# Kernel tuning notes

Measured on AMD Instinct MI355X. Metric: run time of the kernel, lower is better.

## Reference

```python
import jax, jax.numpy as jnp
import numpy as np

M, K, N = 4096, 4096, 11008


def setup_inputs() -> dict:
    key = jax.random.key(0)
    k1, k2, k3 = jax.random.split(key, 3)
    x = jax.random.normal(k1, (M, K), dtype=jnp.float16)
    weight_packed = jax.random.randint(k2, ((K + 1) // 2, N), 0, 256, dtype=jnp.int32)
    weight_scale = jax.random.uniform(k3, (N,), dtype=jnp.float32) * 0.05 + 1e-3
    return {"x": x, "weight_packed": weight_packed, "weight_scale": weight_scale}


def reference(x, weight_packed, weight_scale):
    # Unpack int4 nibbles: low nibble -> even K index, high nibble -> odd K index.
    packed = weight_packed.astype(jnp.uint8)                      # [K//2, N]
    low = (packed & 15).astype(jnp.float32) - 8.0                 # even rows
    high = ((packed >> 4) & 15).astype(jnp.float32) - 8.0         # odd rows
    k = x.shape[-1]
    w = jnp.stack([low, high], axis=1).reshape(-1, low.shape[1])[:k]  # [K, N]
    # Per-output-feature symmetric scale, then fp16 GEMM (matches torch fallback).
    w = (w * weight_scale[None, :]).astype(jnp.float16)
    out = jnp.matmul(x, w)                                        # [M, N] fp16
    return out
```

## Files before the change

kernel.cpp:

```cpp
#include <hip/hip_runtime.h>
#include <hip/hip_fp16.h>
#include <stdint.h>


#define M_DIM 4096
#define K_DIM 4096
#define N_DIM 11008
#define KH    (K_DIM / 2)

#define WS_XH_BYTES  ((size_t)M_DIM * K_DIM * 2)

typedef __attribute__((ext_vector_type(8))) _Float16 f16x8;
typedef __attribute__((ext_vector_type(2))) _Float16 h2;
typedef __attribute__((ext_vector_type(4))) float f32x4;
typedef unsigned short ushortx;

__device__ __forceinline__ unsigned pack_f16_pair(float lo, float hi) {
    return __builtin_bit_cast(unsigned, __builtin_amdgcn_cvt_pkrtz(lo, hi));
}

__device__ __forceinline__ unsigned dq_pair(unsigned v) {
    unsigned c = (v & 0xFu) | ((v << 12) & 0x000F0000u) | 0x64006400u;
    h2 r = __builtin_bit_cast(h2, c) + __builtin_bit_cast(h2, 0xE408E408u);
    return __builtin_bit_cast(unsigned, r);
}

__device__ __forceinline__ void gld_lds16(const void* g, void* l) {
    __builtin_amdgcn_global_load_lds(
        (const __attribute__((address_space(1))) unsigned int*)g,
        (__attribute__((address_space(3))) unsigned int*)l,
        16, 0, 0);
}

__global__ void __launch_bounds__(256) cvt_x_kernel(
    const float* __restrict__ X, unsigned short* __restrict__ Xh)
{
    size_t i = ((size_t)blockIdx.x * 256 + threadIdx.x) * 8;
    float4 a = *(const float4*)(X + i);
    float4 b = *(const float4*)(X + i + 4);
    uint4 o = make_uint4(pack_f16_pair(a.x, a.y), pack_f16_pair(a.z, a.w),
                         pack_f16_pair(b.x, b.y), pack_f16_pair(b.z, b.w));
    *(uint4*)(Xh + i) = o;
}

__global__ void __launch_bounds__(256) dqt_kernel(
    const int* __restrict__ WP, unsigned* __restrict__ Wt)
{
    __shared__ unsigned Lt[64][65];
    const int t = threadIdx.x;
    const int n0 = blockIdx.x * 64;
    const int r0 = blockIdx.y * 64;
    const int g = t >> 6, l = t & 63;
#pragma unroll
    for (int i = 0; i < 16; ++i) {
        const int r = r0 + g * 16 + i;
        Lt[l][g * 16 + i] = dq_pair((unsigned)WP[(size_t)r * N_DIM + n0 + l]);
    }
    __syncthreads();
    const int nr = t >> 2, sg = t & 3;
    unsigned* dst = Wt + (size_t)(n0 + nr) * KH + r0 + sg * 16;
#pragma unroll
    for (int c = 0; c < 4; ++c) {
        uint4 v = make_uint4(Lt[nr][sg * 16 + c * 4 + 0], Lt[nr][sg * 16 + c * 4 + 1],
                             Lt[nr][sg * 16 + c * 4 + 2], Lt[nr][sg * 16 + c * 4 + 3]);
        *(uint4*)(dst + c * 4) = v;
    }
}

__global__ void __launch_bounds__(512, 2) qgemm6_kernel(
    const unsigned short* __restrict__ Xh,
    const unsigned*       __restrict__ Wt,
    const float*          __restrict__ WS,
    float*                __restrict__ Out)
{
    __shared__ unsigned short LA[2][2][8192];
    __shared__ unsigned short LB[2][2][8192];

    const int t = threadIdx.x;
    const int w = t >> 6;
    const int l = t & 63;

    const int bid = blockIdx.x;
    const int wg  = (bid & 7) * 86 + (bid >> 3);
    const int by  = wg / 43;
    const int bx  = wg - by * 43;
    const int bm0 = by * 256;
    const int bn0 = bx * 256;

    const int wr = w >> 2;
    const int wc = w & 3;

    f32x4 acc[8][4];
#pragma unroll
    for (int i = 0; i < 8; ++i)
#pragma unroll
        for (int j = 0; j < 4; ++j)
            acc[i][j] = (f32x4){0.f, 0.f, 0.f, 0.f};

    const int cS = (t & 7) ^ ((t >> 3) & 7);
    const unsigned short* gA0 = Xh + (size_t)(bm0 + (t >> 3)) * K_DIM + cS * 8;
    const unsigned*       gB0 = Wt + (size_t)(bn0 + (t >> 3)) * KH + cS * 4;
    const int t8 = t * 8;

#define STAGE_A(buf, h, kt) do {                                              \
    gld_lds16(gA0 + (size_t)((h) * 128) * K_DIM + (size_t)(kt) * 64,          \
              &LA[buf][h][t8]);                                               \
    gld_lds16(gA0 + (size_t)((h) * 128 + 64) * K_DIM + (size_t)(kt) * 64,     \
              &LA[buf][h][4096 + t8]);                                        \
} while (0)

#define STAGE_B(buf, h, kt) do {                                              \
    gld_lds16(gB0 + (size_t)((h) * 128) * KH + (size_t)(kt) * 32,             \
              &LB[buf][h][t8]);                                               \
    gld_lds16(gB0 + (size_t)((h) * 128 + 64) * KH + (size_t)(kt) * 32,        \
              &LB[buf][h][4096 + t8]);                                        \
} while (0)

    const int lq = l >> 4;
    const int lr = l & 15;

    f16x8 bf[4][2];

#define LOAD_BF(buf) do {                                                     \
    _Pragma("unroll")                                                         \
    for (int ni = 0; ni < 4; ++ni) {                                          \
        const int rrow = (wc & 1) * 64 + ni * 16 + lr;                        \
        _Pragma("unroll")                                                     \
        for (int ks = 0; ks < 2; ++ks)                                        \
            bf[ni][ks] = *(const f16x8*)                                      \
                &LB[buf][wc >> 1][rrow * 64 + ((ks * 4 + lq) ^ (rrow & 7)) * 8]; \
    }                                                                         \
} while (0)

#define MFMA_PH(buf, p) do {                                                  \
    f16x8 _af[2][2];                                                          \
    _Pragma("unroll")                                                         \
    for (int mi2 = 0; mi2 < 2; ++mi2) {                                       \
        const int rrow = (2 * (p) + mi2) * 16 + lr;                           \
        _Pragma("unroll")                                                     \
        for (int ks = 0; ks < 2; ++ks)                                        \
            _af[mi2][ks] = *(const f16x8*)                                    \
                &LA[buf][wr][rrow * 64 + ((ks * 4 + lq) ^ (rrow & 7)) * 8];   \
    }                                                                         \
    __builtin_amdgcn_s_setprio(1);                                            \
    _Pragma("unroll")                                                         \
    for (int mi2 = 0; mi2 < 2; ++mi2)                                         \
        _Pragma("unroll")                                                     \
        for (int ni = 0; ni < 4; ++ni)                                        \
            _Pragma("unroll")                                                 \
            for (int ks = 0; ks < 2; ++ks)                                    \
                acc[2 * (p) + mi2][ni] = __builtin_amdgcn_mfma_f32_16x16x32_f16( \
                    _af[mi2][ks], bf[ni][ks], acc[2 * (p) + mi2][ni], 0, 0, 0); \
    __builtin_amdgcn_s_setprio(0);                                            \
} while (0)

#define WAITV(n) asm volatile("s_waitcnt vmcnt(" #n ")" ::: "memory")
#define BAR()    do { asm volatile("" ::: "memory");                          \
                      __builtin_amdgcn_s_barrier();                           \
                      asm volatile("" ::: "memory"); } while (0)

    const int NT = K_DIM / 64;

    STAGE_A(0, 0, 0); STAGE_A(0, 1, 0);
    STAGE_B(0, 0, 0); STAGE_B(0, 1, 0);

    for (int i = 0; i < 31; ++i) {
        const int t1 = 2 * i + 1, t2 = 2 * i + 2;
        BAR(); STAGE_A(1, 0, t1); WAITV(2); BAR();
        LOAD_BF(0); MFMA_PH(0, 0);
        STAGE_A(1, 1, t1); MFMA_PH(0, 1);
        STAGE_B(1, 0, t1); MFMA_PH(0, 2);
        STAGE_B(1, 1, t1); MFMA_PH(0, 3);
        BAR(); STAGE_A(0, 0, t2); WAITV(2); BAR();
        LOAD_BF(1); MFMA_PH(1, 0);
        STAGE_A(0, 1, t2); MFMA_PH(1, 1);
        STAGE_B(0, 0, t2); MFMA_PH(1, 2);
        STAGE_B(0, 1, t2); MFMA_PH(1, 3);
    }
    {
        BAR(); STAGE_A(1, 0, 63); WAITV(2); BAR();
        LOAD_BF(0); MFMA_PH(0, 0);
        STAGE_A(1, 1, 63); MFMA_PH(0, 1);
        STAGE_B(1, 0, 63); MFMA_PH(0, 2);
        STAGE_B(1, 1, 63); MFMA_PH(0, 3);
        BAR(); WAITV(0); BAR();
        LOAD_BF(1); MFMA_PH(1, 0);
        MFMA_PH(1, 1);
        MFMA_PH(1, 2);
        MFMA_PH(1, 3);
    }

#pragma unroll
    for (int ni = 0; ni < 4; ++ni) {
        const int col = bn0 + wc * 64 + ni * 16 + lr;
        const float s = WS[col];
#pragma unroll
        for (int mi = 0; mi < 8; ++mi) {
            const int row = bm0 + wr * 128 + mi * 16 + lq * 4;
#pragma unroll
            for (int i = 0; i < 4; ++i) {
                Out[(size_t)(row + i) * N_DIM + col] = acc[mi][ni][i] * s;
            }
        }
    }
#undef STAGE_A
#undef STAGE_B
#undef LOAD_BF
#undef MFMA_PH
#undef WAITV
#undef BAR
}

extern "C" void kernel_launch(void* const* d_in, const int* in_sizes, int n_in,
                              void* d_out, int out_size, void* d_ws, size_t ws_size,
                              hipStream_t stream) {
    const float* X  = (const float*)d_in[0];
    const int*   WP = (const int*)d_in[1];
    const float* WS = (const float*)d_in[2];
    float*       Out = (float*)d_out;

    unsigned short* Xh = (unsigned short*)d_ws;
    unsigned*       Wt = (unsigned*)((char*)d_ws + WS_XH_BYTES);

    cvt_x_kernel<<<(M_DIM * K_DIM) / (256 * 8), 256, 0, stream>>>(X, Xh);
    dim3 gdq(N_DIM / 64, KH / 64);
    dqt_kernel<<<gdq, 256, 0, stream>>>(WP, Wt);
    dim3 grid((N_DIM / 256) * (M_DIM / 256));
    qgemm6_kernel<<<grid, 512, 0, stream>>>(Xh, Wt, WS, Out);
}
```

Baseline: 475.4 us.

## Restructure GEMM main loop into quadrant MFMA schedule with barrier-interleaved loads

Replaces the four-phase MFMA loop with a quadrant schedule. Each wave loads A and B fragments for half-tiles and issues 16 MFMAs per quadrant, separated by barriers and explicit lgkmcnt waits. Global-to-LDS loads are split into finer chunks placed between quadrants. The block-to-tile mapping also changes so that each XCD owns two M-rows of tiles, which is meant to improve L2 reuse of A. The extra barriers add synchronisation overhead, and the new mapping changes how much B is shared per XCD.

```diff
diff --git a/kernel.cpp b/kernel.cpp
--- a/kernel.cpp
+++ b/kernel.cpp
@@ -13,7 +13,6 @@
 typedef __attribute__((ext_vector_type(8))) _Float16 f16x8;
 typedef __attribute__((ext_vector_type(2))) _Float16 h2;
 typedef __attribute__((ext_vector_type(4))) float f32x4;
-typedef unsigned short ushortx;
 
 __device__ __forceinline__ unsigned pack_f16_pair(float lo, float hi) {
     return __builtin_bit_cast(unsigned, __builtin_amdgcn_cvt_pkrtz(lo, hi));
@@ -67,7 +66,7 @@
     }
 }
 
-__global__ void __launch_bounds__(512, 2) qgemm6_kernel(
+__global__ void __launch_bounds__(512, 2) qgemm7_kernel(
     const unsigned short* __restrict__ Xh,
     const unsigned*       __restrict__ Wt,
     const float*          __restrict__ WS,
@@ -81,9 +80,10 @@
     const int l = t & 63;
 
     const int bid = blockIdx.x;
-    const int wg  = (bid & 7) * 86 + (bid >> 3);
-    const int by  = wg / 43;
-    const int bx  = wg - by * 43;
+    const int xcd = bid & 7;
+    const int i8  = bid >> 3;
+    const int bx  = i8 >> 1;
+    const int by  = (xcd << 1) | (i8 & 1);
     const int bm0 = by * 256;
     const int bn0 = bx * 256;
 
@@ -102,93 +102,106 @@
     const unsigned*       gB0 = Wt + (size_t)(bn0 + (t >> 3)) * KH + cS * 4;
     const int t8 = t * 8;
 
-#define STAGE_A(buf, h, kt) do {                                              \
-    gld_lds16(gA0 + (size_t)((h) * 128) * K_DIM + (size_t)(kt) * 64,          \
-              &LA[buf][h][t8]);                                               \
-    gld_lds16(gA0 + (size_t)((h) * 128 + 64) * K_DIM + (size_t)(kt) * 64,     \
-              &LA[buf][h][4096 + t8]);                                        \
-} while (0)
-
-#define STAGE_B(buf, h, kt) do {                                              \
+#define SB_H(buf, h, kt) do {                                                 \
     gld_lds16(gB0 + (size_t)((h) * 128) * KH + (size_t)(kt) * 32,             \
               &LB[buf][h][t8]);                                               \
     gld_lds16(gB0 + (size_t)((h) * 128 + 64) * KH + (size_t)(kt) * 32,        \
               &LB[buf][h][4096 + t8]);                                        \
 } while (0)
 
+#define SA_C0(buf, kt) do {                                                   \
+    gld_lds16(gA0 + (size_t)(kt) * 64,                  &LA[buf][0][t8]);     \
+    gld_lds16(gA0 + (size_t)128 * K_DIM + (size_t)(kt) * 64, &LA[buf][1][t8]); \
+} while (0)
+
+#define SA_C1(buf, kt) do {                                                   \
+    gld_lds16(gA0 + (size_t)64 * K_DIM + (size_t)(kt) * 64,                   \
+              &LA[buf][0][4096 + t8]);                                        \
+    gld_lds16(gA0 + (size_t)192 * K_DIM + (size_t)(kt) * 64,                  \
+              &LA[buf][1][4096 + t8]);                                        \
+} while (0)
+
     const int lq = l >> 4;
     const int lr = l & 15;
 
-    f16x8 bf[4][2];
-
-#define LOAD_BF(buf) do {                                                     \
+    f16x8 af0[4][2], af1[4][2], bf0[2][2], bf1[2][2];
+
+#define READ_AF(D, MH, ARR) do {                                              \
     _Pragma("unroll")                                                         \
-    for (int ni = 0; ni < 4; ++ni) {                                          \
-        const int rrow = (wc & 1) * 64 + ni * 16 + lr;                        \
+    for (int mi = 0; mi < 4; ++mi) {                                          \
+        const int row = (MH) * 64 + mi * 16 + lr;                             \
         _Pragma("unroll")                                                     \
         for (int ks = 0; ks < 2; ++ks)                                        \
-            bf[ni][ks] = *(const f16x8*)                                      \
-                &LB[buf][wc >> 1][rrow * 64 + ((ks * 4 + lq) ^ (rrow & 7)) * 8]; \
+            ARR[mi][ks] = *(const f16x8*)                                     \
+                &LA[D][wr][row * 64 + (((ks * 4 + lq) ^ (row & 7)) * 8)];     \
     }                                                                         \
 } while (0)
 
-#define MFMA_PH(buf, p) do {                                                  \
-    f16x8 _af[2][2];                                                          \
+#define READ_BF(D, NH, ARR) do {                                              \
     _Pragma("unroll")                                                         \
-    for (int mi2 = 0; mi2 < 2; ++mi2) {                                       \
-        const int rrow = (2 * (p) + mi2) * 16 + lr;                           \
+    for (int n = 0; n < 2; ++n) {                                             \
+        const int row = (wc & 1) * 64 + ((NH) * 2 + n) * 16 + lr;             \
         _Pragma("unroll")                                                     \
         for (int ks = 0; ks < 2; ++ks)                                        \
-            _af[mi2][ks] = *(const f16x8*)                                    \
-                &LA[buf][wr][rrow * 64 + ((ks * 4 + lq) ^ (rrow & 7)) * 8];   \
+            ARR[n][ks] = *(const f16x8*)                                      \
+                &LB[D][wc >> 1][row * 64 + (((ks * 4 + lq) ^ (row & 7)) * 8)]; \
     }                                                                         \
+} while (0)
+
+#define MFMA_Q(MH, NH, AFA, BFA) do {                                         \
     __builtin_amdgcn_s_setprio(1);                                            \
     _Pragma("unroll")                                                         \
-    for (int mi2 = 0; mi2 < 2; ++mi2)                                         \
+    for (int mi = 0; mi < 4; ++mi)                                            \
         _Pragma("unroll")                                                     \
-        for (int ni = 0; ni < 4; ++ni)                                        \
+        for (int n = 0; n < 2; ++n)                                           \
             _Pragma("unroll")                                                 \
             for (int ks = 0; ks < 2; ++ks)                                    \
-                acc[2 * (p) + mi2][ni] = __builtin_amdgcn_mfma_f32_16x16x32_f16( \
-                    _af[mi2][ks], bf[ni][ks], acc[2 * (p) + mi2][ni], 0, 0, 0); \
+                acc[(MH) * 4 + mi][(NH) * 2 + n] =                            \
+                    __builtin_amdgcn_mfma_f32_16x16x32_f16(                   \
+                        AFA[mi][ks], BFA[n][ks],                              \
+                        acc[(MH) * 4 + mi][(NH) * 2 + n], 0, 0, 0);           \
     __builtin_amdgcn_s_setprio(0);                                            \
 } while (0)
 
 #define WAITV(n) asm volatile("s_waitcnt vmcnt(" #n ")" ::: "memory")
-#define BAR()    do { asm volatile("" ::: "memory");                          \
-                      __builtin_amdgcn_s_barrier();                           \
-                      asm volatile("" ::: "memory"); } while (0)
-
-    const int NT = K_DIM / 64;
-
-    STAGE_A(0, 0, 0); STAGE_A(0, 1, 0);
-    STAGE_B(0, 0, 0); STAGE_B(0, 1, 0);
+#define LGKM0()  do { asm volatile("s_waitcnt lgkmcnt(0)" ::: "memory");      \
+                      __builtin_amdgcn_sched_barrier(0); } while (0)
+#define BAR()    __builtin_amdgcn_s_barrier()
+
+#define TILE_FULL(D, KTN) do {                                                \
+    WAITV(2); BAR();                         \
+    READ_AF(D, 0, af0); READ_BF(D, 0, bf0); READ_BF(D, 1, bf1);               \
+    SB_H(D ^ 1, 0, KTN); BAR(); LGKM0();                                      \
+    MFMA_Q(0, 0, af0, bf0); BAR();                                            \
+    SB_H(D ^ 1, 1, KTN); BAR();                                               \
+    MFMA_Q(0, 1, af0, bf1); BAR();                                            \
+    WAITV(4); BAR();                             \
+    SA_C0(D ^ 1, KTN); READ_AF(D, 1, af1); BAR(); LGKM0();                    \
+    MFMA_Q(1, 1, af1, bf1); BAR();                                            \
+    SA_C1(D ^ 1, KTN); BAR();                                                 \
+    MFMA_Q(1, 0, af1, bf0); BAR();                                            \
+} while (0)
+
+#define TILE_LAST(D) do {                                                     \
+    WAITV(2); BAR();                                                          \
+    READ_AF(D, 0, af0); READ_BF(D, 0, bf0); READ_BF(D, 1, bf1);               \
+    BAR(); LGKM0();                                                           \
+    MFMA_Q(0, 0, af0, bf0); BAR();                                            \
+    MFMA_Q(0, 1, af0, bf1); BAR();                                            \
+    WAITV(0); BAR();                                                          \
+    READ_AF(D, 1, af1); BAR(); LGKM0();                                       \
+    MFMA_Q(1, 1, af1, bf1); BAR();                                            \
+    MFMA_Q(1, 0, af1, bf0);                                                   \
+} while (0)
+
+    SB_H(0, 0, 0); SB_H(0, 1, 0); SA_C0(0, 0); SA_C1(0, 0);
 
     for (int i = 0; i < 31; ++i) {
-        const int t1 = 2 * i + 1, t2 = 2 * i + 2;
-        BAR(); STAGE_A(1, 0, t1); WAITV(2); BAR();
-        LOAD_BF(0); MFMA_PH(0, 0);
-        STAGE_A(1, 1, t1); MFMA_PH(0, 1);
-        STAGE_B(1, 0, t1); MFMA_PH(0, 2);
-        STAGE_B(1, 1, t1); MFMA_PH(0, 3);
-        BAR(); STAGE_A(0, 0, t2); WAITV(2); BAR();
-        LOAD_BF(1); MFMA_PH(1, 0);
-        STAGE_A(0, 1, t2); MFMA_PH(1, 1);
-        STAGE_B(0, 0, t2); MFMA_PH(1, 2);
-        STAGE_B(0, 1, t2); MFMA_PH(1, 3);
-    }
-    {
-        BAR(); STAGE_A(1, 0, 63); WAITV(2); BAR();
-        LOAD_BF(0); MFMA_PH(0, 0);
-        STAGE_A(1, 1, 63); MFMA_PH(0, 1);
-        STAGE_B(1, 0, 63); MFMA_PH(0, 2);
-        STAGE_B(1, 1, 63); MFMA_PH(0, 3);
-        BAR(); WAITV(0); BAR();
-        LOAD_BF(1); MFMA_PH(1, 0);
-        MFMA_PH(1, 1);
-        MFMA_PH(1, 2);
-        MFMA_PH(1, 3);
-    }
+        TILE_FULL(0, 2 * i + 1);
+        TILE_FULL(1, 2 * i + 2);
+    }
+    TILE_FULL(0, 63);
+    TILE_LAST(1);
 
 #pragma unroll
     for (int ni = 0; ni < 4; ++ni) {
@@ -203,12 +216,17 @@
             }
         }
     }
-#undef STAGE_A
-#undef STAGE_B
-#undef LOAD_BF
-#undef MFMA_PH
+#undef SB_H
+#undef SA_C0
+#undef SA_C1
+#undef READ_AF
+#undef READ_BF
+#undef MFMA_Q
 #undef WAITV
+#undef LGKM0
 #undef BAR
+#undef TILE_FULL
+#undef TILE_LAST
 }
 
 extern "C" void kernel_launch(void* const* d_in, const int* in_sizes, int n_in,
@@ -226,5 +244,5 @@
     dim3 gdq(N_DIM / 64, KH / 64);
     dqt_kernel<<<gdq, 256, 0, stream>>>(WP, Wt);
     dim3 grid((N_DIM / 256) * (M_DIM / 256));
-    qgemm6_kernel<<<grid, 512, 0, stream>>>(Xh, Wt, WS, Out);
-}
+    qgemm7_kernel<<<grid, 512, 0, stream>>>(Xh, Wt, WS, Out);
+}
```

Result: no change. 474.4 us (-0.2%).
